# Optimization experiments

Hardware: AMD Instinct MI355X
Metric: run time of the kernel (lower is better)

Reference implementation:

```python
import jax, jax.numpy as jnp
import numpy as np

NEG_SLOPE = 0.01  # nn.LeakyReLU default


def gcn_conv(x, src, dst, deg_inv_sqrt, W, b, n_nodes):
    """PyG GCNConv with self-loops already folded into (src, dst, deg_inv_sqrt).
    out = scatter_add(norm_e * (x @ W)[src]) + b, norm_e = d_src^-1/2 * d_dst^-1/2."""
    h = x @ W  # [N, F_out] -- transform first (F_out < F_in saves gather traffic)
    norm = (deg_inv_sqrt[src] * deg_inv_sqrt[dst])[:, None]  # [E, 1]
    msg = h[src] * norm  # [E, F_out]
    return jax.ops.segment_sum(msg, dst, num_segments=n_nodes) + b


def setup_inputs() -> dict:
    key = jax.random.key(0)
    ks = jax.random.split(key, 8)
    N, E, F_IN, F_HID, F_OUT = 50000, 800000, 256, 128, 64
    x = jax.random.normal(ks[0], (N, F_IN), dtype=jnp.float32)
    edge_index = jax.random.randint(ks[1], (2, E), 0, N, dtype=jnp.int64)
    def glorot(k, shape):
        lim = float(np.sqrt(6.0 / (shape[0] + shape[1])))
        return jax.random.uniform(k, shape, jnp.float32, -lim, lim)
    return {
        "x": x,
        "edge_index": edge_index,
        "W1": glorot(ks[2], (F_IN, F_HID)),
        "b1": jnp.zeros((F_HID,), jnp.float32),
        "W_mu": glorot(ks[3], (F_HID, F_OUT)),
        "b_mu": jnp.zeros((F_OUT,), jnp.float32),
        "W_logvar": glorot(ks[4], (F_HID, F_OUT)),
        "b_logvar": jnp.zeros((F_OUT,), jnp.float32),
    }


def reference(x, edge_index, W1, b1, W_mu, b_mu, W_logvar, b_logvar):
    n_nodes = x.shape[0]
    loops = jnp.arange(n_nodes, dtype=edge_index.dtype)
    src = jnp.concatenate([edge_index[0], loops])
    dst = jnp.concatenate([edge_index[1], loops])
    # degree on destination nodes (includes self-loop); >= 1 so rsqrt is safe
    deg = jax.ops.segment_sum(jnp.ones_like(dst, dtype=x.dtype), dst, num_segments=n_nodes)
    deg_inv_sqrt = jax.lax.rsqrt(deg)

    h = gcn_conv(x, src, dst, deg_inv_sqrt, W1, b1, n_nodes)
    h = jax.nn.leaky_relu(h, NEG_SLOPE)
    mu = gcn_conv(h, src, dst, deg_inv_sqrt, W_mu, b_mu, n_nodes)
    logvar = gcn_conv(h, src, dst, deg_inv_sqrt, W_logvar, b_logvar, n_nodes)
    return (mu, logvar)
```

## Files before the change

### kernel.cpp

```cpp
#include <hip/hip_runtime.h>

#define NEG_SLOPE 0.01f
#define EPB 4096
#define NB_SHIFT 8
#define PAD_SHIFT 13

typedef __attribute__((ext_vector_type(8))) short bf16x8;
typedef __attribute__((ext_vector_type(4))) float floatx4;

__device__ __forceinline__ short f2bf(float f) {
    union { float f; unsigned u; } v; v.f = f;
    unsigned u = v.u;
    u += 0x7FFF + ((u >> 16) & 1);
    return (short)(u >> 16);
}
__device__ __forceinline__ float bf2f(short s) {
    union { unsigned u; float f; } v;
    v.u = ((unsigned)(unsigned short)s) << 16;
    return v.f;
}

__launch_bounds__(256)
__global__ void pack_weights(const float* __restrict__ W1, const float* __restrict__ Wmu,
                             const float* __restrict__ Wlv,
                             short* __restrict__ w1f, short* __restrict__ wcatf,
                             int* __restrict__ bcur, int K) {
    if (blockIdx.x == 192) {
        if (threadIdx.x < K) bcur[threadIdx.x] = 0;
        return;
    }
    int i = blockIdx.x * 256 + threadIdx.x;
    if (i < 128 * 256) {
        int j  = i & 7;
        int ln = (i >> 3) & 15;
        int q  = (i >> 7) & 3;
        int t  = (i >> 9) & 7;
        int kb = i >> 12;
        int n = t * 16 + ln;
        int k = kb * 32 + q * 8 + j;
        w1f[i] = f2bf(W1[k * 128 + n]);
    } else {
        int i2 = i - 128 * 256;
        int j  = i2 & 7;
        int ln = (i2 >> 3) & 15;
        int q  = (i2 >> 7) & 3;
        int t  = (i2 >> 9) & 7;
        int kb = i2 >> 12;
        int n = t * 16 + ln;
        int k = kb * 32 + q * 8 + j;
        wcatf[i2] = f2bf((n < 64) ? Wmu[k * 64 + n] : Wlv[k * 64 + (n - 64)]);
    }
}

__device__ __forceinline__ void gemm1_body64(int blk, int tid, const float* __restrict__ Ap,
                                             const short* __restrict__ Bfrag,
                                             short* __restrict__ C, int M) {
    int w = tid >> 6;
    int lane = tid & 63;
    int ln = lane & 15;
    int q  = lane >> 4;
    int row0 = blk * 64 + w * 16;

    int r0 = row0 + ln;
    int r0c = (r0 < M) ? r0 : (M - 1);
    const float* aF = Ap + (size_t)r0c * 256 + q * 8;
    const short* bLane = Bfrag + lane * 8;

    floatx4 acc[8];
    #pragma unroll
    for (int t = 0; t < 8; t++) acc[t] = (floatx4){0.f, 0.f, 0.f, 0.f};

    #pragma unroll
    for (int kb = 0; kb < 8; kb++) {
        int kt = kb * 32;
        float4 x0 = *(const float4*)(aF + kt);
        float4 x1 = *(const float4*)(aF + kt + 4);
        bf16x8 a;
        a[0] = f2bf(x0.x); a[1] = f2bf(x0.y); a[2] = f2bf(x0.z); a[3] = f2bf(x0.w);
        a[4] = f2bf(x1.x); a[5] = f2bf(x1.y); a[6] = f2bf(x1.z); a[7] = f2bf(x1.w);
        bf16x8 bF[8];
        #pragma unroll
        for (int t = 0; t < 8; t++)
            bF[t] = *(const bf16x8*)(bLane + (size_t)(kb * 8 + t) * 512);
        #pragma unroll
        for (int t = 0; t < 8; t++)
            acc[t] = __builtin_amdgcn_mfma_f32_16x16x32_bf16(a, bF[t], acc[t], 0, 0, 0);
    }

    #pragma unroll
    for (int reg = 0; reg < 4; reg++) {
        int r = row0 + q * 4 + reg;
        if (r < M) {
            #pragma unroll
            for (int t = 0; t < 8; t++)
                C[(size_t)r * 128 + t * 16 + ln] = f2bf(acc[t][reg]);
        }
    }
}

__launch_bounds__(256)
__global__ void scatter_gemm1(const int* __restrict__ src, const int* __restrict__ dst,
                              int E, int B, int G64, int* __restrict__ bcur,
                              unsigned* __restrict__ bucketed,
                              const float* __restrict__ x, const short* __restrict__ w1f,
                              short* __restrict__ z1, int M) {
    __shared__ int lh[256];
    __shared__ int lofs[256];
    __shared__ int gbase[256];
    __shared__ unsigned srt[EPB];
    __shared__ int waveTot[4];
    __shared__ int waveOff[4];
    int bid = blockIdx.x;
    int tid = threadIdx.x;
    if (bid < G64) {
        gemm1_body64(bid, tid, x, w1f, z1, M);
    } else {
        int sbid = bid - G64;
        lh[tid] = 0;
        __syncthreads();
        int lo = sbid * EPB, hi = min(lo + EPB, E);
        for (int e = lo + tid; e < hi; e += 256)
            atomicAdd(&lh[dst[e] >> NB_SHIFT], 1);
        __syncthreads();
        int v = lh[tid];
        int lane = tid & 63, wave = tid >> 6;
        int s = v;
        #pragma unroll
        for (int o = 1; o < 64; o <<= 1) {
            int t = __shfl_up(s, o);
            if (lane >= o) s += t;
        }
        if (lane == 63) waveTot[wave] = s;
        __syncthreads();
        if (tid == 0) {
            int acc = 0;
            #pragma unroll
            for (int w = 0; w < 4; w++) { waveOff[w] = acc; acc += waveTot[w]; }
        }
        __syncthreads();
        int excl = s - v + waveOff[wave];
        lofs[tid] = excl;
        if (v) gbase[tid] = (tid << PAD_SHIFT) + atomicAdd(&bcur[tid], v);
        __syncthreads();
        lh[tid] = excl;
        __syncthreads();
        for (int e = lo + tid; e < hi; e += 256) {
            int d = dst[e];
            unsigned rec = (unsigned)(src[e] & 0xFFFF) | ((unsigned)d << 16);
            int p = atomicAdd(&lh[d >> NB_SHIFT], 1);
            srt[p] = rec;
        }
        __syncthreads();
        int cnt = hi - lo;
        for (int p = tid; p < cnt; p += 256) {
            unsigned r = srt[p];
            int k = r >> 24;
            int pos = gbase[k] + (p - lofs[k]);
            if (pos < ((k + 1) << PAD_SHIFT))
                bucketed[pos] = r;
        }
    }
}

__global__ void fill_csr_deg(const unsigned* __restrict__ bucketed,
                             const int* __restrict__ bcur,
                             int* __restrict__ row_ptr, int* __restrict__ row_end,
                             float* __restrict__ dis,
                             unsigned short* __restrict__ csr_src, int N) {
    __shared__ int cnt[256];
    __shared__ int rp[256];
    __shared__ int waveTot[4];
    __shared__ int waveOff[4];
    __shared__ unsigned short lcsr[8192];
    int k = blockIdx.x;
    int tid = threadIdx.x;
    int base = k << NB_SHIFT;
    cnt[tid] = 0;
    __syncthreads();
    int lo = k << PAD_SHIFT;
    int m = bcur[k];
    if (m > 8192) m = 8192;
    int hi = lo + m;
    for (int e = lo + tid; e < hi; e += 256)
        atomicAdd(&cnt[(bucketed[e] >> 16) & 255], 1);
    __syncthreads();
    int v = cnt[tid];
    int lane = tid & 63, wave = tid >> 6;
    int s = v;
    #pragma unroll
    for (int o = 1; o < 64; o <<= 1) {
        int t = __shfl_up(s, o);
        if (lane >= o) s += t;
    }
    if (lane == 63) waveTot[wave] = s;
    __syncthreads();
    if (tid == 0) {
        int acc = 0;
        #pragma unroll
        for (int w = 0; w < 4; w++) { waveOff[w] = acc; acc += waveTot[w]; }
    }
    __syncthreads();
    int excl = s - v + waveOff[wave];
    rp[tid] = excl;
    int node = base + tid;
    if (node < N) {
        row_ptr[node] = lo + excl;
        row_end[node] = lo + excl + v;
        dis[node] = rsqrtf(1.0f + (float)v);
    }
    __syncthreads();
    for (int e = lo + tid; e < hi; e += 256) {
        unsigned sd = bucketed[e];
        int p = atomicAdd(&rp[(sd >> 16) & 255], 1);
        lcsr[p] = (unsigned short)(sd & 0xFFFFu);
    }
    __syncthreads();
    for (int i = tid; i < m; i += 256) csr_src[lo + i] = lcsr[i];
}

template<bool WEIGHTED>
__device__ __forceinline__ void agg_quarter(const short* __restrict__ zb,
                                            const unsigned short* __restrict__ csr_src,
                                            const float* __restrict__ dis,
                                            int start, int end, int qbase, int fl,
                                            float acc[8]) {
    for (int bse = start; bse < end; bse += 16) {
        int n = end - bse; n = (n > 16) ? 16 : n;
        int idx = (int)csr_src[bse + ((fl < n) ? fl : 0)];
        float dl = WEIGHTED ? dis[idx] : 1.f;
        #pragma unroll
        for (int e = 0; e < 16; e += 8) {
            if (e >= n) break;
            bf16x8 r[8];
            float wt[8];
            #pragma unroll
            for (int k = 0; k < 8; ++k) {
                int ee = e + k;
                int s0 = __shfl(idx, qbase + ee);
                float we = WEIGHTED ? __shfl(dl, qbase + ee) : 1.f;
                wt[k] = (ee < n) ? we : 0.f;
                r[k] = *(const bf16x8*)(zb + (size_t)s0 * 128);
            }
            #pragma unroll
            for (int k = 0; k < 8; ++k)
                #pragma unroll
                for (int t = 0; t < 8; t++)
                    acc[t] = fmaf(wt[k], bf2f(r[k][t]), acc[t]);
        }
    }
}

__launch_bounds__(256)
__global__ void agg1_gemm2(const short* __restrict__ z1, const int* __restrict__ row_ptr,
                           const int* __restrict__ row_end,
                           const unsigned short* __restrict__ csr_src,
                           const float* __restrict__ dis, const float* __restrict__ b1,
                           const short* __restrict__ wcatf,
                           short* __restrict__ z2, int N) {
    __shared__ short htile[16 * 128];
    int tid = threadIdx.x;
    int w = tid >> 6;
    int lane = tid & 63;
    int qi = lane >> 4;
    int fl = lane & 15;
    int fo = fl * 8;
    int qbase = qi * 16;
    int base = blockIdx.x * 16;
    int local = w * 4 + qi;
    int node = base + local;

    short* hrow = &htile[(local * 128 + fo) ^ ((local & 7) * 8)];
    bf16x8 ov = (bf16x8){0, 0, 0, 0, 0, 0, 0, 0};
    if (node < N) {
        const short* zb = z1 + fo;
        int start = row_ptr[node], end = row_end[node];
        float acc[8];
        #pragma unroll
        for (int t = 0; t < 8; t++) acc[t] = 0.f;
        agg_quarter<true>(zb, csr_src, dis, start, end, qbase, fl, acc);
        float dn = dis[node];
        bf16x8 zs = *(const bf16x8*)(zb + (size_t)node * 128);
        #pragma unroll
        for (int t = 0; t < 8; t++) acc[t] = fmaf(dn, bf2f(zs[t]), acc[t]);
        #pragma unroll
        for (int t = 0; t < 8; t++) {
            float v = fmaf(dn, acc[t], b1[fo + t]);
            v = (v > 0.f) ? v : NEG_SLOPE * v;
            ov[t] = f2bf(v);
        }
    }
    *(bf16x8*)hrow = ov;
    __syncthreads();

    int r0 = fl;
    const short* bLane = wcatf + lane * 8;

    floatx4 acc[2];
    #pragma unroll
    for (int t = 0; t < 2; t++) acc[t] = (floatx4){0.f, 0.f, 0.f, 0.f};

    #pragma unroll
    for (int kb = 0; kb < 4; kb++) {
        int k0 = kb * 32 + qi * 8;
        bf16x8 aF = *(const bf16x8*)&htile[(r0 * 128 + k0) ^ ((r0 & 7) * 8)];
        #pragma unroll
        for (int t = 0; t < 2; t++) {
            int tt = w * 2 + t;
            bf16x8 bF = *(const bf16x8*)(bLane + (size_t)(kb * 8 + tt) * 512);
            acc[t] = __builtin_amdgcn_mfma_f32_16x16x32_bf16(aF, bF, acc[t], 0, 0, 0);
        }
    }

    #pragma unroll
    for (int reg = 0; reg < 4; reg++) {
        int gr = base + qi * 4 + reg;
        if (gr < N) {
            float s = dis[gr];
            #pragma unroll
            for (int t = 0; t < 2; t++)
                z2[(size_t)gr * 128 + (w * 2 + t) * 16 + fl] = f2bf(s * acc[t][reg]);
        }
    }
}

__launch_bounds__(256)
__global__ void agg_layer2(const short* __restrict__ zp, const int* __restrict__ row_ptr,
                           const int* __restrict__ row_end,
                           const unsigned short* __restrict__ csr_src,
                           const float* __restrict__ dis, const float* __restrict__ b_mu,
                           const float* __restrict__ b_lv, float* __restrict__ out, int N) {
    int tid = threadIdx.x;
    int w = tid >> 6;
    int lane = tid & 63;
    int qi = lane >> 4;
    int fl = lane & 15;
    int fo = fl * 8;
    int qbase = qi * 16;
    int node = blockIdx.x * 16 + w * 4 + qi;
    if (node >= N) return;

    const short* zb = zp + fo;
    int start = row_ptr[node], end = row_end[node];
    float acc[8];
    #pragma unroll
    for (int t = 0; t < 8; t++) acc[t] = 0.f;
    agg_quarter<false>(zb, csr_src, nullptr, start, end, qbase, fl, acc);
    bf16x8 zs = *(const bf16x8*)(zb + (size_t)node * 128);
    #pragma unroll
    for (int t = 0; t < 8; t++) acc[t] += bf2f(zs[t]);

    float d = dis[node];
    float r[8];
    if (fl < 8) {
        #pragma unroll
        for (int t = 0; t < 8; t++) r[t] = fmaf(d, acc[t], b_mu[fo + t]);
        float* p = out + (size_t)node * 64 + fo;
        *(float4*)p       = make_float4(r[0], r[1], r[2], r[3]);
        *(float4*)(p + 4) = make_float4(r[4], r[5], r[6], r[7]);
    } else {
        #pragma unroll
        for (int t = 0; t < 8; t++) r[t] = fmaf(d, acc[t], b_lv[fo - 64 + t]);
        float* p = out + (size_t)N * 64 + (size_t)node * 64 + (fo - 64);
        *(float4*)p       = make_float4(r[0], r[1], r[2], r[3]);
        *(float4*)(p + 4) = make_float4(r[4], r[5], r[6], r[7]);
    }
}


extern "C" void kernel_launch(void* const* d_in, const int* in_sizes, int n_in,
                              void* d_out, int out_size, void* d_ws, size_t ws_size,
                              hipStream_t stream) {
    const float* x   = (const float*)d_in[0];
    const int*   ei  = (const int*)d_in[1];
    const float* W1  = (const float*)d_in[2];
    const float* b1  = (const float*)d_in[3];
    const float* Wmu = (const float*)d_in[4];
    const float* bmu = (const float*)d_in[5];
    const float* Wlv = (const float*)d_in[6];
    const float* blv = (const float*)d_in[7];
    float* out = (float*)d_out;

    const int F_IN = 256;
    int N = in_sizes[0] / F_IN;
    int E = in_sizes[1] / 2;
    const int* e_src = ei;
    const int* e_dst = ei + E;

    int B = (E + EPB - 1) / EPB;
    int K = (N + 255) >> NB_SHIFT;
    int G64 = (N + 63) / 64;
    int G2 = (N + 15) / 16;

    char* ws = (char*)d_ws;
    size_t off = 0;
    auto carve = [&](size_t bytes) -> void* {
        void* p = ws + off;
        off += (bytes + 255) & ~(size_t)255;
        return p;
    };
    int*      row_end  = (int*)   carve((size_t)N * 4);
    int*      row_ptr  = (int*)   carve((size_t)N * 4);
    float*    dis      = (float*) carve((size_t)N * 4);
    unsigned short* csr_src = (unsigned short*)carve((size_t)K << PAD_SHIFT << 1);
    short*    bufA     = (short*) carve((size_t)N * 128 * 2);
    short*    bufB     = (short*) carve((size_t)N * 128 * 2);
    short*    w1f      = (short*) carve(128 * 256 * 2);
    short*    wcatf    = (short*) carve(128 * 128 * 2);
    int*      bcur     = (int*)   carve((size_t)K * 4);
    unsigned* bucketed = (unsigned*)carve((size_t)K << PAD_SHIFT << 2);

    hipLaunchKernelGGL(pack_weights, dim3(193), dim3(256), 0, stream,
                       W1, Wmu, Wlv, w1f, wcatf, bcur, K);
    hipLaunchKernelGGL(scatter_gemm1, dim3(G64 + B), dim3(256), 0, stream,
                       e_src, e_dst, E, B, G64, bcur, bucketed, x, w1f, bufA, N);
    hipLaunchKernelGGL(fill_csr_deg, dim3(K), dim3(256), 0, stream,
                       bucketed, bcur, row_ptr, row_end, dis, csr_src, N);
    hipLaunchKernelGGL(agg1_gemm2, dim3(G2), dim3(256), 0, stream,
                       bufA, row_ptr, row_end, csr_src, dis, b1, wcatf, bufB, N);
    hipLaunchKernelGGL(agg_layer2, dim3(G2), dim3(256), 0, stream,
                       bufB, row_ptr, row_end, csr_src, dis, bmu, blv, out, N);
}
```

Measured before the change: 195.5 us.

## Split fused scatter/GEMM kernel, widen CSR fill blocks, shrink aggregation batch

Breaks the combined edge-scatter plus first GEMM kernel into a standalone edge-scatter kernel and a separate GEMM kernel launched after the CSR fill. Each kernel can then get its own register and occupancy profile instead of sharing the heavier one. The CSR fill kernel now runs with 512 threads per block, and the scan stays on the first 256. The aggregation inner loop gathers 4 rows per batch instead of 8, which lowers register pressure but leaves fewer loads in flight. The cost is one extra kernel launch and the loss of overlap between the GEMM and the scatter.

```diff
diff --git a/kernel.cpp b/kernel.cpp
--- a/kernel.cpp
+++ b/kernel.cpp
@@ -52,58 +52,10 @@
     }
 }
 
-__device__ __forceinline__ void gemm1_body64(int blk, int tid, const float* __restrict__ Ap,
-                                             const short* __restrict__ Bfrag,
-                                             short* __restrict__ C, int M) {
-    int w = tid >> 6;
-    int lane = tid & 63;
-    int ln = lane & 15;
-    int q  = lane >> 4;
-    int row0 = blk * 64 + w * 16;
-
-    int r0 = row0 + ln;
-    int r0c = (r0 < M) ? r0 : (M - 1);
-    const float* aF = Ap + (size_t)r0c * 256 + q * 8;
-    const short* bLane = Bfrag + lane * 8;
-
-    floatx4 acc[8];
-    #pragma unroll
-    for (int t = 0; t < 8; t++) acc[t] = (floatx4){0.f, 0.f, 0.f, 0.f};
-
-    #pragma unroll
-    for (int kb = 0; kb < 8; kb++) {
-        int kt = kb * 32;
-        float4 x0 = *(const float4*)(aF + kt);
-        float4 x1 = *(const float4*)(aF + kt + 4);
-        bf16x8 a;
-        a[0] = f2bf(x0.x); a[1] = f2bf(x0.y); a[2] = f2bf(x0.z); a[3] = f2bf(x0.w);
-        a[4] = f2bf(x1.x); a[5] = f2bf(x1.y); a[6] = f2bf(x1.z); a[7] = f2bf(x1.w);
-        bf16x8 bF[8];
-        #pragma unroll
-        for (int t = 0; t < 8; t++)
-            bF[t] = *(const bf16x8*)(bLane + (size_t)(kb * 8 + t) * 512);
-        #pragma unroll
-        for (int t = 0; t < 8; t++)
-            acc[t] = __builtin_amdgcn_mfma_f32_16x16x32_bf16(a, bF[t], acc[t], 0, 0, 0);
-    }
-
-    #pragma unroll
-    for (int reg = 0; reg < 4; reg++) {
-        int r = row0 + q * 4 + reg;
-        if (r < M) {
-            #pragma unroll
-            for (int t = 0; t < 8; t++)
-                C[(size_t)r * 128 + t * 16 + ln] = f2bf(acc[t][reg]);
-        }
-    }
-}
-
 __launch_bounds__(256)
-__global__ void scatter_gemm1(const int* __restrict__ src, const int* __restrict__ dst,
-                              int E, int B, int G64, int* __restrict__ bcur,
-                              unsigned* __restrict__ bucketed,
-                              const float* __restrict__ x, const short* __restrict__ w1f,
-                              short* __restrict__ z1, int M) {
+__global__ void scatter_edges(const int* __restrict__ src, const int* __restrict__ dst,
+                              int E, int* __restrict__ bcur,
+                              unsigned* __restrict__ bucketed) {
     __shared__ int lh[256];
     __shared__ int lofs[256];
     __shared__ int gbase[256];
@@ -112,56 +64,52 @@
     __shared__ int waveOff[4];
     int bid = blockIdx.x;
     int tid = threadIdx.x;
-    if (bid < G64) {
-        gemm1_body64(bid, tid, x, w1f, z1, M);
-    } else {
-        int sbid = bid - G64;
-        lh[tid] = 0;
-        __syncthreads();
-        int lo = sbid * EPB, hi = min(lo + EPB, E);
-        for (int e = lo + tid; e < hi; e += 256)
-            atomicAdd(&lh[dst[e] >> NB_SHIFT], 1);
-        __syncthreads();
-        int v = lh[tid];
-        int lane = tid & 63, wave = tid >> 6;
-        int s = v;
-        #pragma unroll
-        for (int o = 1; o < 64; o <<= 1) {
-            int t = __shfl_up(s, o);
-            if (lane >= o) s += t;
-        }
-        if (lane == 63) waveTot[wave] = s;
-        __syncthreads();
-        if (tid == 0) {
-            int acc = 0;
-            #pragma unroll
-            for (int w = 0; w < 4; w++) { waveOff[w] = acc; acc += waveTot[w]; }
-        }
-        __syncthreads();
-        int excl = s - v + waveOff[wave];
-        lofs[tid] = excl;
-        if (v) gbase[tid] = (tid << PAD_SHIFT) + atomicAdd(&bcur[tid], v);
-        __syncthreads();
-        lh[tid] = excl;
-        __syncthreads();
-        for (int e = lo + tid; e < hi; e += 256) {
-            int d = dst[e];
-            unsigned rec = (unsigned)(src[e] & 0xFFFF) | ((unsigned)d << 16);
-            int p = atomicAdd(&lh[d >> NB_SHIFT], 1);
-            srt[p] = rec;
-        }
-        __syncthreads();
-        int cnt = hi - lo;
-        for (int p = tid; p < cnt; p += 256) {
-            unsigned r = srt[p];
-            int k = r >> 24;
-            int pos = gbase[k] + (p - lofs[k]);
-            if (pos < ((k + 1) << PAD_SHIFT))
-                bucketed[pos] = r;
-        }
-    }
-}
-
+    lh[tid] = 0;
+    __syncthreads();
+    int lo = bid * EPB, hi = min(lo + EPB, E);
+    for (int e = lo + tid; e < hi; e += 256)
+        atomicAdd(&lh[dst[e] >> NB_SHIFT], 1);
+    __syncthreads();
+    int v = lh[tid];
+    int lane = tid & 63, wave = tid >> 6;
+    int s = v;
+    #pragma unroll
+    for (int o = 1; o < 64; o <<= 1) {
+        int t = __shfl_up(s, o);
+        if (lane >= o) s += t;
+    }
+    if (lane == 63) waveTot[wave] = s;
+    __syncthreads();
+    if (tid == 0) {
+        int acc = 0;
+        #pragma unroll
+        for (int w = 0; w < 4; w++) { waveOff[w] = acc; acc += waveTot[w]; }
+    }
+    __syncthreads();
+    int excl = s - v + waveOff[wave];
+    lofs[tid] = excl;
+    if (v) gbase[tid] = (tid << PAD_SHIFT) + atomicAdd(&bcur[tid], v);
+    __syncthreads();
+    lh[tid] = excl;
+    __syncthreads();
+    for (int e = lo + tid; e < hi; e += 256) {
+        int d = dst[e];
+        unsigned rec = (unsigned)(src[e] & 0xFFFF) | ((unsigned)d << 16);
+        int p = atomicAdd(&lh[d >> NB_SHIFT], 1);
+        srt[p] = rec;
+    }
+    __syncthreads();
+    int cnt = hi - lo;
+    for (int p = tid; p < cnt; p += 256) {
+        unsigned r = srt[p];
+        int k = r >> 24;
+        int pos = gbase[k] + (p - lofs[k]);
+        if (pos < ((k + 1) << PAD_SHIFT))
+            bucketed[pos] = r;
+    }
+}
+
+__launch_bounds__(512)
 __global__ void fill_csr_deg(const unsigned* __restrict__ bucketed,
                              const int* __restrict__ bcur,
                              int* __restrict__ row_ptr, int* __restrict__ row_end,
@@ -175,24 +123,28 @@
     int k = blockIdx.x;
     int tid = threadIdx.x;
     int base = k << NB_SHIFT;
-    cnt[tid] = 0;
+    if (tid < 256) cnt[tid] = 0;
     __syncthreads();
     int lo = k << PAD_SHIFT;
     int m = bcur[k];
     if (m > 8192) m = 8192;
     int hi = lo + m;
-    for (int e = lo + tid; e < hi; e += 256)
+    for (int e = lo + tid; e < hi; e += 512)
         atomicAdd(&cnt[(bucketed[e] >> 16) & 255], 1);
     __syncthreads();
-    int v = cnt[tid];
     int lane = tid & 63, wave = tid >> 6;
-    int s = v;
-    #pragma unroll
-    for (int o = 1; o < 64; o <<= 1) {
-        int t = __shfl_up(s, o);
-        if (lane >= o) s += t;
-    }
-    if (lane == 63) waveTot[wave] = s;
+    int v = 0, excl = 0;
+    if (tid < 256) {
+        v = cnt[tid];
+        int s = v;
+        #pragma unroll
+        for (int o = 1; o < 64; o <<= 1) {
+            int t = __shfl_up(s, o);
+            if (lane >= o) s += t;
+        }
+        if (lane == 63) waveTot[wave] = s;
+        excl = s - v;
+    }
     __syncthreads();
     if (tid == 0) {
         int acc = 0;
@@ -200,22 +152,71 @@
         for (int w = 0; w < 4; w++) { waveOff[w] = acc; acc += waveTot[w]; }
     }
     __syncthreads();
-    int excl = s - v + waveOff[wave];
-    rp[tid] = excl;
-    int node = base + tid;
-    if (node < N) {
-        row_ptr[node] = lo + excl;
-        row_end[node] = lo + excl + v;
-        dis[node] = rsqrtf(1.0f + (float)v);
-    }
-    __syncthreads();
-    for (int e = lo + tid; e < hi; e += 256) {
+    if (tid < 256) {
+        excl += waveOff[wave];
+        rp[tid] = excl;
+        int node = base + tid;
+        if (node < N) {
+            row_ptr[node] = lo + excl;
+            row_end[node] = lo + excl + v;
+            dis[node] = rsqrtf(1.0f + (float)v);
+        }
+    }
+    __syncthreads();
+    for (int e = lo + tid; e < hi; e += 512) {
         unsigned sd = bucketed[e];
         int p = atomicAdd(&rp[(sd >> 16) & 255], 1);
         lcsr[p] = (unsigned short)(sd & 0xFFFFu);
     }
     __syncthreads();
-    for (int i = tid; i < m; i += 256) csr_src[lo + i] = lcsr[i];
+    for (int i = tid; i < m; i += 512) csr_src[lo + i] = lcsr[i];
+}
+
+__launch_bounds__(256)
+__global__ void gemm1_kernel(const float* __restrict__ Ap, const short* __restrict__ Bfrag,
+                             short* __restrict__ C, int M) {
+    int tid = threadIdx.x;
+    int w = tid >> 6;
+    int lane = tid & 63;
+    int ln = lane & 15;
+    int q  = lane >> 4;
+    int row0 = blockIdx.x * 64 + w * 16;
+
+    int r0 = row0 + ln;
+    int r0c = (r0 < M) ? r0 : (M - 1);
+    const float* aF = Ap + (size_t)r0c * 256 + q * 8;
+    const short* bLane = Bfrag + lane * 8;
+
+    floatx4 acc[8];
+    #pragma unroll
+    for (int t = 0; t < 8; t++) acc[t] = (floatx4){0.f, 0.f, 0.f, 0.f};
+
+    #pragma unroll
+    for (int kb = 0; kb < 8; kb++) {
+        int kt = kb * 32;
+        float4 x0 = *(const float4*)(aF + kt);
+        float4 x1 = *(const float4*)(aF + kt + 4);
+        bf16x8 a;
+        a[0] = f2bf(x0.x); a[1] = f2bf(x0.y); a[2] = f2bf(x0.z); a[3] = f2bf(x0.w);
+        a[4] = f2bf(x1.x); a[5] = f2bf(x1.y); a[6] = f2bf(x1.z); a[7] = f2bf(x1.w);
+        bf16x8 bF[8];
+        #pragma unroll
+        for (int t = 0; t < 8; t++)
+            bF[t] = *(const bf16x8*)(bLane + (size_t)(kb * 8 + t) * 512);
+        #pragma unroll
+        for (int t = 0; t < 8; t++)
+            acc[t] = __builtin_amdgcn_mfma_f32_16x16x32_bf16(a, bF[t], acc[t], 0, 0, 0);
+    }
+
+    #pragma unroll
+    for (int reg = 0; reg < 4; reg++) {
+        int r = row0 + q * 4 + reg;
+        if (r < M) {
+            #pragma unroll
+            for (int t = 0; t < 8; t++)
+                C[(size_t)r * 128 + t * 16 + ln] = f2bf(acc[t][reg]);
+        }
+    }
 }
 
 template<bool WEIGHTED>
@@ -228,24 +229,19 @@
         int n = end - bse; n = (n > 16) ? 16 : n;
         int idx = (int)csr_src[bse + ((fl < n) ? fl : 0)];
         float dl = WEIGHTED ? dis[idx] : 1.f;
-        #pragma unroll
-        for (int e = 0; e < 16; e += 8) {
+        for (int e = 0; e < 16; e += 4) {
             if (e >= n) break;
-            bf16x8 r[8];
-            float wt[8];
             #pragma unroll
-            for (int k = 0; k < 8; ++k) {
+            for (int k = 0; k < 4; ++k) {
                 int ee = e + k;
                 int s0 = __shfl(idx, qbase + ee);
                 float we = WEIGHTED ? __shfl(dl, qbase + ee) : 1.f;
-                wt[k] = (ee < n) ? we : 0.f;
-                r[k] = *(const bf16x8*)(zb + (size_t)s0 * 128);
-            }
-            #pragma unroll
-            for (int k = 0; k < 8; ++k)
+                if (ee >= n) we = 0.f;
+                bf16x8 zv = *(const bf16x8*)(zb + (size_t)s0 * 128);
                 #pragma unroll
                 for (int t = 0; t < 8; t++)
-                    acc[t] = fmaf(wt[k], bf2f(r[k][t]), acc[t]);
+                    acc[t] = fmaf(we, bf2f(zv[t]), acc[t]);
+            }
         }
     }
 }
@@ -411,10 +407,12 @@
 
     hipLaunchKernelGGL(pack_weights, dim3(193), dim3(256), 0, stream,
                        W1, Wmu, Wlv, w1f, wcatf, bcur, K);
-    hipLaunchKernelGGL(scatter_gemm1, dim3(G64 + B), dim3(256), 0, stream,
-                       e_src, e_dst, E, B, G64, bcur, bucketed, x, w1f, bufA, N);
-    hipLaunchKernelGGL(fill_csr_deg, dim3(K), dim3(256), 0, stream,
+    hipLaunchKernelGGL(scatter_edges, dim3(B), dim3(256), 0, stream,
+                       e_src, e_dst, E, bcur, bucketed);
+    hipLaunchKernelGGL(fill_csr_deg, dim3(K), dim3(512), 0, stream,
                        bucketed, bcur, row_ptr, row_end, dis, csr_src, N);
+    hipLaunchKernelGGL(gemm1_kernel, dim3(G64), dim3(256), 0, stream,
+                       x, w1f, bufA, N);
     hipLaunchKernelGGL(agg1_gemm2, dim3(G2), dim3(256), 0, stream,
                        bufA, row_ptr, row_end, csr_src, dis, b1, wcatf, bufB, N);
     hipLaunchKernelGGL(agg_layer2, dim3(G2), dim3(256), 0, stream,
```

After: 204.1 us. +4.4%, slower.
